# Kernel optimization log

Hardware: AMD Instinct MI355X
Metric: run time of the kernel (lower is better)

## Reference

```python
import jax, jax.numpy as jnp
import numpy as np

B_SCALE = 1.3195079565048218  # per_level_scale
N_LEVELS = 4                  # kernel hardcodes 4 levels
F = 4                         # kernel hardcodes 4 features per level
BASE = 32.0                   # kernel hardcodes base resolution 32
MAX_PARAMS = 2 ** 19
N_POINTS = 2097152


def _level_meta():
    offsets = []
    off = 0
    for i in range(N_LEVELS):
        res = int(np.ceil(BASE * np.exp(i * np.log(B_SCALE)) - 1.0)) + 1
        p = res ** 3
        p = p if p % 8 == 0 else ((p + 7) // 8) * 8
        p = min(MAX_PARAMS, p)
        offsets.append(off)
        off += p
    return offsets, off

OFFSETS, TOTAL_PARAMS = _level_meta()
TOTAL_HASH_SIZE = TOTAL_PARAMS * F  # 2772480


def setup_inputs() -> dict:
    key = jax.random.key(0)
    k1, k2 = jax.random.split(key)
    # scale to [0, 0.9) so all 8 corner indices stay inside each level's grid
    positions = jax.random.uniform(k1, (N_POINTS, 3), dtype=jnp.float32) * 0.9
    # original init: uniform(-1e-4, 1e-4); small random values
    table = jax.random.normal(k2, (TOTAL_HASH_SIZE,), dtype=jnp.float32) * 1e-4
    return {"positions": positions, "table": table}


def _encode(positions, table):
    tab = table.reshape(-1, F)  # [total_params, 4]
    n = positions.shape[0]
    outs = []
    for level in range(N_LEVELS):
        scale = BASE * (B_SCALE ** level) - 1.0
        res = int(np.ceil(scale)) + 1
        pos = positions * scale + 0.5            # [n,3]
        grid = jnp.floor(pos)
        frac = pos - grid                         # trilinear fractions
        grid = grid.astype(jnp.int32)
        acc = jnp.zeros((n, F), positions.dtype)
        for c in range(8):  # 8 corners of the cell
            w = jnp.ones((n,), positions.dtype)
            idx = jnp.zeros((n,), jnp.int32)
            stride = 1
            for d in range(3):
                if (c >> d) & 1:
                    coord = grid[:, d] + 1
                    w = w * frac[:, d]
                else:
                    coord = grid[:, d]
                    w = w * (1.0 - frac[:, d])
                idx = idx + coord * stride
                stride *= res
            acc = acc + w[:, None] * tab[OFFSETS[level] + idx]
        outs.append(acc)
    return jnp.concatenate(outs, axis=1)  # [n, 16]


def reference(positions, table):
    return _encode(positions, table)
```

## Files before the change

kernel.cpp:

```cpp
#include <hip/hip_runtime.h>
#include <math.h>


#define NBINS        512
#define BIN_SCALE    (8.0f / 0.9f)
#define SCAT_THREADS 512
#define PTS_PER_BLK  4096
#define SCAT_ITERS   (PTS_PER_BLK / SCAT_THREADS)
#define CAP          4608

#define ENC_THREADS  512
#define ENC_HALF     (CAP / 2)

#define D0 6
#define D1 7
#define D2 9
#define D3 11
#define A0 0
#define A1 (A0 + D0*D0*D0)
#define A2 (A1 + D1*D1*D1)
#define A3 (A2 + D2*D2*D2)
#define LDS_TOT (A3 + D3*D3*D3)

typedef float vfloat4 __attribute__((ext_vector_type(4)));

__device__ __forceinline__ int bin_of(float x, float y, float z) {
    int bx = (int)(x * BIN_SCALE); bx = bx < 0 ? 0 : (bx > 7 ? 7 : bx);
    int by = (int)(y * BIN_SCALE); by = by < 0 ? 0 : (by > 7 ? 7 : by);
    int bz = (int)(z * BIN_SCALE); bz = bz < 0 ? 0 : (bz > 7 ? 7 : bz);
    return bx | (by << 3) | (bz << 6);
}


__global__ __launch_bounds__(SCAT_THREADS) void scatter_cap_kernel(
    const float* __restrict__ pos, int n, int* __restrict__ cursor,
    float4* __restrict__ sorted, int bin_stride)
{
    __shared__ float4         lds_rec[PTS_PER_BLK];
    __shared__ unsigned short lds_bin[PTS_PER_BLK];
    __shared__ int lds_hist[NBINS];
    __shared__ int lds_lbase[NBINS];
    __shared__ int lds_gbase[NBINS];
    __shared__ int lds_wsum[8];

    int tid = threadIdx.x;
    long base = (long)blockIdx.x * PTS_PER_BLK;
    lds_hist[tid] = 0;
    __syncthreads();

    float px[SCAT_ITERS], py[SCAT_ITERS], pz[SCAT_ITERS];
    int br[SCAT_ITERS];
#pragma unroll
    for (int j = 0; j < SCAT_ITERS; ++j) {
        long p = base + j * SCAT_THREADS + tid;
        int packed = -1;
        if (p < n) {
            float x = pos[3 * p], y = pos[3 * p + 1], z = pos[3 * p + 2];
            px[j] = x; py[j] = y; pz[j] = z;
            int b = bin_of(x, y, z);
            int r = atomicAdd(&lds_hist[b], 1);
            packed = (r << 9) | b;
        }
        br[j] = packed;
    }
    __syncthreads();

    int lane = tid & 63, wid = tid >> 6;
    int cntb = lds_hist[tid];
    int v = cntb;
#pragma unroll
    for (int off = 1; off < 64; off <<= 1) {
        int u = __shfl_up(v, off, 64);
        if (lane >= off) v += u;
    }
    if (lane == 63) lds_wsum[wid] = v;
    __syncthreads();
    if (tid < 8) {
        int w = lds_wsum[tid];
#pragma unroll
        for (int off = 1; off < 8; off <<= 1) {
            int u = __shfl_up(w, off, 8);
            if (tid >= off) w += u;
        }
        lds_wsum[tid] = w;
    }
    if (cntb) lds_gbase[tid] = atomicAdd(&cursor[tid], cntb);
    __syncthreads();
    int wbase = wid ? lds_wsum[wid - 1] : 0;
    int excl  = wbase + v - cntb;
    lds_lbase[tid] = excl;
    __syncthreads();

#pragma unroll
    for (int j = 0; j < SCAT_ITERS; ++j) {
        if (br[j] < 0) continue;
        int b = br[j] & (NBINS - 1);
        int r = br[j] >> 9;
        int s = lds_lbase[b] + r;
        long p = base + j * SCAT_THREADS + tid;
        lds_rec[s] = make_float4(px[j], py[j], pz[j], __int_as_float((int)p));
        lds_bin[s] = (unsigned short)b;
    }
    __syncthreads();

    long rem = (long)n - base;
    int tot = rem >= PTS_PER_BLK ? PTS_PER_BLK : (rem > 0 ? (int)rem : 0);
    for (int s = tid; s < tot; s += SCAT_THREADS) {
        float4 rec = lds_rec[s];
        int b = lds_bin[s];
        int off_in_bin = s - lds_lbase[b];
        long slot = (long)b * bin_stride + lds_gbase[b] + off_in_bin;
        sorted[slot] = rec;
    }
}

template<int D>
__device__ __forceinline__ void stage_win(
    float4* __restrict__ dst, const float4* __restrict__ tab,
    int off, int res, int Bx, int By, int Bz, int tid)
{
    const int DD = D * D, DDD = D * D * D;
    for (int e = tid; e < DDD; e += ENC_THREADS) {
        int iz  = e / DD;
        int rem = e - iz * DD;
        int iy  = rem / D;
        int ix  = rem - iy * D;
        int gx = Bx + ix; gx = gx < 0 ? 0 : (gx > res - 1 ? res - 1 : gx);
        int gy = By + iy; gy = gy < 0 ? 0 : (gy > res - 1 ? res - 1 : gy);
        int gz = Bz + iz; gz = gz < 0 ? 0 : (gz > res - 1 ? res - 1 : gz);
        dst[e] = tab[off + gx + gy * res + gz * res * res];
    }
}

template<int D>
__device__ __forceinline__ float4 interp_one(
    const float4* __restrict__ lds, const float4* __restrict__ tab,
    float x, float y, float z, float scale, int res, int off,
    int Bx, int By, int Bz)
{
    float hx = x * scale + 0.5f, hy = y * scale + 0.5f, hz = z * scale + 0.5f;
    float fx = floorf(hx), fy = floorf(hy), fz = floorf(hz);
    float wx = hx - fx, wy = hy - fy, wz = hz - fz;
    float ox = 1.0f - wx, oy = 1.0f - wy, oz = 1.0f - wz;
    int gx = (int)fx, gy = (int)fy, gz = (int)fz;
    int lx = gx - Bx, ly = gy - By, lz = gz - Bz;
    float4 acc = make_float4(0.f, 0.f, 0.f, 0.f);
    if ((unsigned)lx <= (unsigned)(D - 2) &&
        (unsigned)ly <= (unsigned)(D - 2) &&
        (unsigned)lz <= (unsigned)(D - 2)) {
        int basei = (lz * D + ly) * D + lx;
#pragma unroll
        for (int c = 0; c < 8; ++c) {
            int   idx = basei + ((c & 1) ? 1 : 0) + ((c & 2) ? D : 0) + ((c & 4) ? D * D : 0);
            float w   = ((c & 1) ? wx : ox) * ((c & 2) ? wy : oy) * ((c & 4) ? wz : oz);
            float4 v  = lds[idx];
            acc.x += w * v.x; acc.y += w * v.y; acc.z += w * v.z; acc.w += w * v.w;
        }
    } else {
        int res2  = res * res;
        int basei = off + gx + gy * res + gz * res2;
#pragma unroll
        for (int c = 0; c < 8; ++c) {
            int   idx = basei + ((c & 1) ? 1 : 0) + ((c & 2) ? res : 0) + ((c & 4) ? res2 : 0);
            float w   = ((c & 1) ? wx : ox) * ((c & 2) ? wy : oy) * ((c & 4) ? wz : oz);
            float4 v  = tab[idx];
            acc.x += w * v.x; acc.y += w * v.y; acc.z += w * v.z; acc.w += w * v.w;
        }
    }
    return acc;
}

__global__ __launch_bounds__(ENC_THREADS) void encode_bin_kernel(
    const float4* __restrict__ sorted,
    const int* __restrict__ cursor,
    const float4* __restrict__ tab,
    float4* __restrict__ out,
    float s0, float s1, float s2, float s3,
    int r0, int r1, int r2, int r3,
    int o0, int o1, int o2, int o3)
{
    __shared__ float4 lds[LDS_TOT];

    int nb = (int)gridDim.x;
    int lb = (int)blockIdx.x;
    lb = (lb & 7) * (nb >> 3) + (lb >> 3);

    int b = lb >> 1;
    int k = lb & 1;
    int cnt = cursor[b];

    int begin = k * ENC_HALF;
    int end   = k ? cnt : (cnt < ENC_HALF ? cnt : ENC_HALF);
    if (begin >= end) return;

    int tid = threadIdx.x;

    int bx = b & 7, by = (b >> 3) & 7, bz = b >> 6;
    float lox = bx * 0.1125f, loy = by * 0.1125f, loz = bz * 0.1125f;

    int B0x = (int)floorf(lox * s0 + 0.5f), B0y = (int)floorf(loy * s0 + 0.5f), B0z = (int)floorf(loz * s0 + 0.5f);
    int B1x = (int)floorf(lox * s1 + 0.5f), B1y = (int)floorf(loy * s1 + 0.5f), B1z = (int)floorf(loz * s1 + 0.5f);
    int B2x = (int)floorf(lox * s2 + 0.5f), B2y = (int)floorf(loy * s2 + 0.5f), B2z = (int)floorf(loz * s2 + 0.5f);
    int B3x = (int)floorf(lox * s3 + 0.5f), B3y = (int)floorf(loy * s3 + 0.5f), B3z = (int)floorf(loz * s3 + 0.5f);

    stage_win<D0>(lds + A0, tab, o0, r0, B0x, B0y, B0z, tid);
    stage_win<D1>(lds + A1, tab, o1, r1, B1x, B1y, B1z, tid);
    stage_win<D2>(lds + A2, tab, o2, r2, B2x, B2y, B2z, tid);
    stage_win<D3>(lds + A3, tab, o3, r3, B3x, B3y, B3z, tid);
    __syncthreads();

    const float4* sbin = sorted + (long)b * CAP;
    int jmax = CAP - 1;
    int iters = (end - begin + ENC_THREADS - 1) / ENC_THREADS;

    int local = begin + tid;
    vfloat4 rv = __builtin_nontemporal_load(
        (const vfloat4*)&sbin[local <= jmax ? local : jmax]);

    for (int it = 0; it < iters; ++it) {
        int nloc = local + ENC_THREADS;
        vfloat4 nx = rv;
        if (it + 1 < iters)
            nx = __builtin_nontemporal_load(
                (const vfloat4*)&sbin[nloc <= jmax ? nloc : jmax]);
        if (local < end) {
            float x = rv.x, y = rv.y, z = rv.z;
            int p = __float_as_int(rv.w);
            float4* op = out + (long)p * 4;
            float4 a0 = interp_one<D0>(lds + A0, tab, x, y, z, s0, r0, o0, B0x, B0y, B0z);
            float4 a1 = interp_one<D1>(lds + A1, tab, x, y, z, s1, r1, o1, B1x, B1y, B1z);
            float4 a2 = interp_one<D2>(lds + A2, tab, x, y, z, s2, r2, o2, B2x, B2y, B2z);
            float4 a3 = interp_one<D3>(lds + A3, tab, x, y, z, s3, r3, o3, B3x, B3y, B3z);
            op[0] = a0; op[1] = a1; op[2] = a2; op[3] = a3;
        }
        rv = nx;
        local = nloc;
    }
}


__device__ __forceinline__ void interp_levels(
    float4 rec, const float4* __restrict__ tab, float4* __restrict__ o,
    float s0, float s1, float s2, float s3,
    int r0, int r1, int r2, int r3,
    int o0, int o1, int o2, int o3)
{
    float scales[4] = { s0, s1, s2, s3 };
    int   ress[4]   = { r0, r1, r2, r3 };
    int   offs[4]   = { o0, o1, o2, o3 };
#pragma unroll
    for (int l = 0; l < 4; ++l) {
        float scale = scales[l];
        int   res   = ress[l];
        int   off   = offs[l];
        float hx = rec.x * scale + 0.5f;
        float hy = rec.y * scale + 0.5f;
        float hz = rec.z * scale + 0.5f;
        float gx = floorf(hx), gy = floorf(hy), gz = floorf(hz);
        float wx = hx - gx,   wy = hy - gy,   wz = hz - gz;
        float ox = 1.0f - wx, oy = 1.0f - wy, oz = 1.0f - wz;
        int res2 = res * res;
        int base = off + (int)gx + (int)gy * res + (int)gz * res2;
        float4 acc = make_float4(0.f, 0.f, 0.f, 0.f);
#pragma unroll
        for (int c = 0; c < 8; ++c) {
            int   idx = base + ((c & 1) ? 1 : 0) + ((c & 2) ? res : 0) + ((c & 4) ? res2 : 0);
            float w   = ((c & 1) ? wx : ox) * ((c & 2) ? wy : oy) * ((c & 4) ? wz : oz);
            float4 v  = tab[idx];
            acc.x += w * v.x; acc.y += w * v.y; acc.z += w * v.z; acc.w += w * v.w;
        }
        o[l] = acc;
    }
}


__global__ __launch_bounds__(SCAT_THREADS) void hist_kernel(
    const float* __restrict__ pos, int n, int* __restrict__ hist)
{
    __shared__ int lh[NBINS];
    int tid = threadIdx.x;
    lh[tid] = 0;
    __syncthreads();
    long base = (long)blockIdx.x * PTS_PER_BLK;
#pragma unroll
    for (int j = 0; j < SCAT_ITERS; ++j) {
        long p = base + j * SCAT_THREADS + tid;
        if (p < n) {
            float x = pos[3 * p], y = pos[3 * p + 1], z = pos[3 * p + 2];
            atomicAdd(&lh[bin_of(x, y, z)], 1);
        }
    }
    __syncthreads();
    int c = lh[tid];
    if (c) atomicAdd(&hist[tid], c);
}

__global__ __launch_bounds__(256) void scan_kernel(
    const int* __restrict__ hist, int* __restrict__ cursor)
{
    __shared__ int partials[256];
    int t = threadIdx.x;
    int a = hist[2 * t], b = hist[2 * t + 1];
    int sum = a + b;
    partials[t] = sum;
    __syncthreads();
    for (int off = 1; off < 256; off <<= 1) {
        int v = (t >= off) ? partials[t - off] : 0;
        __syncthreads();
        partials[t] += v;
        __syncthreads();
    }
    int base = partials[t] - sum;
    cursor[2 * t]     = base;
    cursor[2 * t + 1] = base + a;
}

__global__ __launch_bounds__(256) void encode_kernel(
    const float4* __restrict__ sorted, const float4* __restrict__ tab,
    float4* __restrict__ out, int n,
    float s0, float s1, float s2, float s3,
    int r0, int r1, int r2, int r3,
    int o0, int o1, int o2, int o3)
{
    int j = blockIdx.x * blockDim.x + threadIdx.x;
    if (j >= n) return;
    vfloat4 rv = __builtin_nontemporal_load((const vfloat4*)&sorted[j]);
    float4 rec = make_float4(rv.x, rv.y, rv.z, rv.w);
    int p = __float_as_int(rec.w);
    interp_levels(rec, tab, out + (long)p * 4,
                  s0, s1, s2, s3, r0, r1, r2, r3, o0, o1, o2, o3);
}

__global__ __launch_bounds__(256) void encode_direct_kernel(
    const float* __restrict__ pos, const float4* __restrict__ tab,
    float4* __restrict__ out, int n_points,
    float s0, float s1, float s2, float s3,
    int r0, int r1, int r2, int r3,
    int o0, int o1, int o2, int o3)
{
    int t = blockIdx.x * blockDim.x + threadIdx.x;
    int p = t >> 2;
    if (p >= n_points) return;
    int l = t & 3;
    float scale = (l == 0) ? s0 : (l == 1) ? s1 : (l == 2) ? s2 : s3;
    int   res   = (l == 0) ? r0 : (l == 1) ? r1 : (l == 2) ? r2 : r3;
    int   off   = (l == 0) ? o0 : (l == 1) ? o1 : (l == 2) ? o2 : o3;
    float px = pos[3 * p], py = pos[3 * p + 1], pz = pos[3 * p + 2];
    float hx = px * scale + 0.5f, hy = py * scale + 0.5f, hz = pz * scale + 0.5f;
    float gx = floorf(hx), gy = floorf(hy), gz = floorf(hz);
    float wx = hx - gx, wy = hy - gy, wz = hz - gz;
    float ox = 1.f - wx, oy = 1.f - wy, oz = 1.f - wz;
    int res2 = res * res;
    int base = off + (int)gx + (int)gy * res + (int)gz * res2;
    float4 acc = make_float4(0.f, 0.f, 0.f, 0.f);
#pragma unroll
    for (int c = 0; c < 8; ++c) {
        int   idx = base + ((c & 1) ? 1 : 0) + ((c & 2) ? res : 0) + ((c & 4) ? res2 : 0);
        float w   = ((c & 1) ? wx : ox) * ((c & 2) ? wy : oy) * ((c & 4) ? wz : oz);
        float4 v  = tab[idx];
        acc.x += w * v.x; acc.y += w * v.y; acc.z += w * v.z; acc.w += w * v.w;
    }
    out[t] = acc;
}

extern "C" void kernel_launch(void* const* d_in, const int* in_sizes, int n_in,
                              void* d_out, int out_size, void* d_ws, size_t ws_size,
                              hipStream_t stream) {
    const float*  positions = (const float*)d_in[0];
    const float4* table     = (const float4*)d_in[1];
    float4*       out       = (float4*)d_out;
    int n = in_sizes[0] / 3;

    const double B_SCALE = 1.3195079565048218;
    const double BASE = 32.0;
    const long   MAX_PARAMS = 1L << 19;
    float scales[4]; int res[4], offs[4];
    long off = 0;
    for (int l = 0; l < 4; ++l) {
        double s = BASE * pow(B_SCALE, (double)l) - 1.0;
        scales[l] = (float)s;
        int r = (int)ceil(s) + 1;
        res[l] = r;
        offs[l] = (int)off;
        long pcount = (long)r * r * r;
        if (pcount % 8 != 0) pcount = (pcount + 7) / 8 * 8;
        if (pcount > MAX_PARAMS) pcount = MAX_PARAMS;
        off += pcount;
    }

    size_t need_cap   = (size_t)NBINS * sizeof(int) + (size_t)NBINS * CAP * 16;
    size_t need_exact = (size_t)NBINS * sizeof(int) * 2 + (size_t)n * 16;

    if (ws_size >= need_cap && n <= NBINS * (CAP - 512)) {
        int*    cursor = (int*)d_ws;
        float4* sorted = (float4*)(cursor + NBINS);

        int grid_pts = (n + PTS_PER_BLK - 1) / PTS_PER_BLK;
        int grid_enc = NBINS * 2;

        (void)hipMemsetAsync(cursor, 0, NBINS * sizeof(int), stream);
        scatter_cap_kernel<<<grid_pts, SCAT_THREADS, 0, stream>>>(
            positions, n, cursor, sorted, CAP);
        encode_bin_kernel<<<grid_enc, ENC_THREADS, 0, stream>>>(
            sorted, cursor, table, out,
            scales[0], scales[1], scales[2], scales[3],
            res[0], res[1], res[2], res[3],
            offs[0], offs[1], offs[2], offs[3]);
    } else if (ws_size >= need_exact) {
        int*    hist   = (int*)d_ws;
        int*    cursor = hist + NBINS;
        float4* sorted = (float4*)(cursor + NBINS);

        int grid_pts = (n + PTS_PER_BLK - 1) / PTS_PER_BLK;
        int grid_enc = (n + 255) / 256;

        (void)hipMemsetAsync(hist, 0, NBINS * sizeof(int), stream);
        hist_kernel<<<grid_pts, SCAT_THREADS, 0, stream>>>(positions, n, hist);
        scan_kernel<<<1, 256, 0, stream>>>(hist, cursor);
        scatter_cap_kernel<<<grid_pts, SCAT_THREADS, 0, stream>>>(
            positions, n, cursor, sorted, 0);
        encode_kernel<<<grid_enc, 256, 0, stream>>>(
            sorted, table, out, n,
            scales[0], scales[1], scales[2], scales[3],
            res[0], res[1], res[2], res[3],
            offs[0], offs[1], offs[2], offs[3]);
    } else {
        long n_threads = 4L * n;
        long grid = (n_threads + 255) / 256;
        encode_direct_kernel<<<dim3((unsigned)grid), dim3(256), 0, stream>>>(
            positions, table, out, n,
            scales[0], scales[1], scales[2], scales[3],
            res[0], res[1], res[2], res[3],
            offs[0], offs[1], offs[2], offs[3]);
    }
}
```

Measured before the change: 230.1 us.

## Sort points within each wavefront by finest-level cell before LDS interpolation

Each wavefront runs a 64-lane bitonic sort over the points it holds, keyed by their level-3 cell inside the bin window, then shuffles the coordinates so neighbouring lanes read nearby LDS entries. The aim is fewer LDS bank conflicts and more coherent gathers in interp_one. The encode grid also changes from two half-bin blocks of 512 threads to one 1024-thread block per bin. The sort adds about 21 shuffle-and-compare stages per iteration, and the larger blocks cut the number of blocks and may reduce occupancy.

```diff
diff --git a/kernel.cpp b/kernel.cpp
--- a/kernel.cpp
+++ b/kernel.cpp
@@ -9,8 +9,7 @@
 #define SCAT_ITERS   (PTS_PER_BLK / SCAT_THREADS)
 #define CAP          4608
 
-#define ENC_THREADS  512
-#define ENC_HALF     (CAP / 2)
+#define ENC_THREADS  1024
 
 #define D0 6
 #define D1 7
@@ -21,6 +20,8 @@
 #define A2 (A1 + D1*D1*D1)
 #define A3 (A2 + D2*D2*D2)
 #define LDS_TOT (A3 + D3*D3*D3)
+
+#define KEY_SENTINEL 2047u
 
 typedef float vfloat4 __attribute__((ext_vector_type(4)));
 
@@ -182,18 +183,12 @@
     __shared__ float4 lds[LDS_TOT];
 
     int nb = (int)gridDim.x;
-    int lb = (int)blockIdx.x;
-    lb = (lb & 7) * (nb >> 3) + (lb >> 3);
-
-    int b = lb >> 1;
-    int k = lb & 1;
+    int b  = (int)blockIdx.x;
+    b = (b & 7) * (nb >> 3) + (b >> 3);
+
     int cnt = cursor[b];
-
-    int begin = k * ENC_HALF;
-    int end   = k ? cnt : (cnt < ENC_HALF ? cnt : ENC_HALF);
-    if (begin >= end) return;
-
     int tid = threadIdx.x;
+    int lane = tid & 63;
 
     int bx = b & 7, by = (b >> 3) & 7, bz = b >> 6;
     float lox = bx * 0.1125f, loy = by * 0.1125f, loz = bz * 0.1125f;
@@ -209,11 +204,15 @@
     stage_win<D3>(lds + A3, tab, o3, r3, B3x, B3y, B3z, tid);
     __syncthreads();
 
+    if (cnt == 0) return;
+
+    int iters = (cnt + ENC_THREADS - 1) / ENC_THREADS;
     const float4* sbin = sorted + (long)b * CAP;
     int jmax = CAP - 1;
-    int iters = (end - begin + ENC_THREADS - 1) / ENC_THREADS;
-
-    int local = begin + tid;
+
+    float cx = lox + 0.05625f, cy = loy + 0.05625f, cz = loz + 0.05625f;
+
+    int local = tid;
     vfloat4 rv = __builtin_nontemporal_load(
         (const vfloat4*)&sbin[local <= jmax ? local : jmax]);
 
@@ -223,14 +222,46 @@
         if (it + 1 < iters)
             nx = __builtin_nontemporal_load(
                 (const vfloat4*)&sbin[nloc <= jmax ? nloc : jmax]);
-        if (local < end) {
-            float x = rv.x, y = rv.y, z = rv.z;
-            int p = __float_as_int(rv.w);
+
+        bool valid = (local < cnt);
+        float x = valid ? rv.x : cx;
+        float y = valid ? rv.y : cy;
+        float z = valid ? rv.z : cz;
+        float pw = rv.w;
+
+        int kx = (int)floorf(x * s3 + 0.5f) - B3x; kx = kx < 0 ? 0 : (kx > D3 - 1 ? D3 - 1 : kx);
+        int ky = (int)floorf(y * s3 + 0.5f) - B3y; ky = ky < 0 ? 0 : (ky > D3 - 1 ? D3 - 1 : ky);
+        int kz = (int)floorf(z * s3 + 0.5f) - B3z; kz = kz < 0 ? 0 : (kz > D3 - 1 ? D3 - 1 : kz);
+        unsigned key = valid ? (unsigned)((kz * D3 + ky) * D3 + kx) : KEY_SENTINEL;
+        unsigned comp = (key << 6) | (unsigned)lane;
+
+#pragma unroll
+        for (int k = 2; k <= 64; k <<= 1) {
+#pragma unroll
+            for (int j = k >> 1; j >= 1; j >>= 1) {
+                unsigned o = (unsigned)__shfl_xor((int)comp, j, 64);
+                bool up    = ((lane & k) == 0);
+                bool lower = ((lane & j) == 0);
+                unsigned mn = comp < o ? comp : o;
+                unsigned mx = comp < o ? o : comp;
+                comp = (lower == up) ? mn : mx;
+            }
+        }
+        int src = (int)(comp & 63u);
+        x  = __shfl(x,  src, 64);
+        y  = __shfl(y,  src, 64);
+        z  = __shfl(z,  src, 64);
+        pw = __shfl(pw, src, 64);
+        valid = ((comp >> 6) != KEY_SENTINEL);
+
+        float4 a0 = interp_one<D0>(lds + A0, tab, x, y, z, s0, r0, o0, B0x, B0y, B0z);
+        float4 a1 = interp_one<D1>(lds + A1, tab, x, y, z, s1, r1, o1, B1x, B1y, B1z);
+        float4 a2 = interp_one<D2>(lds + A2, tab, x, y, z, s2, r2, o2, B2x, B2y, B2z);
+        float4 a3 = interp_one<D3>(lds + A3, tab, x, y, z, s3, r3, o3, B3x, B3y, B3z);
+
+        if (valid) {
+            int p = __float_as_int(pw);
             float4* op = out + (long)p * 4;
-            float4 a0 = interp_one<D0>(lds + A0, tab, x, y, z, s0, r0, o0, B0x, B0y, B0z);
-            float4 a1 = interp_one<D1>(lds + A1, tab, x, y, z, s1, r1, o1, B1x, B1y, B1z);
-            float4 a2 = interp_one<D2>(lds + A2, tab, x, y, z, s2, r2, o2, B2x, B2y, B2z);
-            float4 a3 = interp_one<D3>(lds + A3, tab, x, y, z, s3, r3, o3, B3x, B3y, B3z);
             op[0] = a0; op[1] = a1; op[2] = a2; op[3] = a3;
         }
         rv = nx;
@@ -396,12 +427,11 @@
         float4* sorted = (float4*)(cursor + NBINS);
 
         int grid_pts = (n + PTS_PER_BLK - 1) / PTS_PER_BLK;
-        int grid_enc = NBINS * 2;
 
         (void)hipMemsetAsync(cursor, 0, NBINS * sizeof(int), stream);
         scatter_cap_kernel<<<grid_pts, SCAT_THREADS, 0, stream>>>(
             positions, n, cursor, sorted, CAP);
-        encode_bin_kernel<<<grid_enc, ENC_THREADS, 0, stream>>>(
+        encode_bin_kernel<<<NBINS, ENC_THREADS, 0, stream>>>(
             sorted, cursor, table, out,
             scales[0], scales[1], scales[2], scales[3],
             res[0], res[1], res[2], res[3],
```

After: 230.4 us. Within noise of the previous version (+0.1%).

## Vectorize scatter position loads and use one 1024-thread encode block per bin

Applied to the files above, without the earlier changes.

The scatter kernel now has each thread load four consecutive points as three float4 vector loads, replacing scalar strided loads, which should improve coalescing on the positions read. The encode kernel goes from two 512-thread blocks per bin (each handling half of the bin) to a single 1024-thread block per bin. This halves the number of times each bin's table window is staged into LDS. The trade-off is fewer blocks in flight and a larger block that may limit occupancy, and the vector path assumes 16-byte alignment of the positions buffer.

```diff
diff --git a/kernel.cpp b/kernel.cpp
--- a/kernel.cpp
+++ b/kernel.cpp
@@ -7,10 +7,11 @@
 #define SCAT_THREADS 512
 #define PTS_PER_BLK  4096
 #define SCAT_ITERS   (PTS_PER_BLK / SCAT_THREADS)
+#define PTS_PER_PASS (SCAT_THREADS * 4)
+#define NPASS        (PTS_PER_BLK / PTS_PER_PASS)
 #define CAP          4608
 
-#define ENC_THREADS  512
-#define ENC_HALF     (CAP / 2)
+#define ENC_THREADS  1024
 
 #define D0 6
 #define D1 7
@@ -48,20 +49,40 @@
     lds_hist[tid] = 0;
     __syncthreads();
 
-    float px[SCAT_ITERS], py[SCAT_ITERS], pz[SCAT_ITERS];
-    int br[SCAT_ITERS];
-#pragma unroll
-    for (int j = 0; j < SCAT_ITERS; ++j) {
-        long p = base + j * SCAT_THREADS + tid;
-        int packed = -1;
-        if (p < n) {
-            float x = pos[3 * p], y = pos[3 * p + 1], z = pos[3 * p + 2];
-            px[j] = x; py[j] = y; pz[j] = z;
-            int b = bin_of(x, y, z);
-            int r = atomicAdd(&lds_hist[b], 1);
-            packed = (r << 9) | b;
-        }
-        br[j] = packed;
+    float px[4 * NPASS], py[4 * NPASS], pz[4 * NPASS];
+    int br[4 * NPASS];
+#pragma unroll
+    for (int pass = 0; pass < NPASS; ++pass) {
+        long p0 = base + (long)pass * PTS_PER_PASS + 4 * tid;
+        int ii = pass * 4;
+        if (p0 + 4 <= n) {
+            const float4* v = (const float4*)(pos + 3 * p0);
+            float4 A = v[0], B = v[1], C = v[2];
+            px[ii+0]=A.x; py[ii+0]=A.y; pz[ii+0]=A.z;
+            px[ii+1]=A.w; py[ii+1]=B.x; pz[ii+1]=B.y;
+            px[ii+2]=B.z; py[ii+2]=B.w; pz[ii+2]=C.x;
+            px[ii+3]=C.y; py[ii+3]=C.z; pz[ii+3]=C.w;
+#pragma unroll
+            for (int q = 0; q < 4; ++q) {
+                int b = bin_of(px[ii+q], py[ii+q], pz[ii+q]);
+                int r = atomicAdd(&lds_hist[b], 1);
+                br[ii+q] = (r << 9) | b;
+            }
+        } else {
+#pragma unroll
+            for (int q = 0; q < 4; ++q) {
+                long p = p0 + q;
+                int packed = -1;
+                if (p < n) {
+                    float x = pos[3*p], y = pos[3*p+1], z = pos[3*p+2];
+                    px[ii+q]=x; py[ii+q]=y; pz[ii+q]=z;
+                    int b = bin_of(x, y, z);
+                    int r = atomicAdd(&lds_hist[b], 1);
+                    packed = (r << 9) | b;
+                }
+                br[ii+q] = packed;
+            }
+        }
     }
     __syncthreads();
 
@@ -92,13 +113,13 @@
     __syncthreads();
 
 #pragma unroll
-    for (int j = 0; j < SCAT_ITERS; ++j) {
-        if (br[j] < 0) continue;
-        int b = br[j] & (NBINS - 1);
-        int r = br[j] >> 9;
+    for (int ii = 0; ii < 4 * NPASS; ++ii) {
+        if (br[ii] < 0) continue;
+        int b = br[ii] & (NBINS - 1);
+        int r = br[ii] >> 9;
         int s = lds_lbase[b] + r;
-        long p = base + j * SCAT_THREADS + tid;
-        lds_rec[s] = make_float4(px[j], py[j], pz[j], __int_as_float((int)p));
+        long p = base + (long)(ii >> 2) * PTS_PER_PASS + 4 * tid + (ii & 3);
+        lds_rec[s] = make_float4(px[ii], py[ii], pz[ii], __int_as_float((int)p));
         lds_bin[s] = (unsigned short)b;
     }
     __syncthreads();
@@ -182,17 +203,10 @@
     __shared__ float4 lds[LDS_TOT];
 
     int nb = (int)gridDim.x;
-    int lb = (int)blockIdx.x;
-    lb = (lb & 7) * (nb >> 3) + (lb >> 3);
-
-    int b = lb >> 1;
-    int k = lb & 1;
+    int b  = (int)blockIdx.x;
+    b = (b & 7) * (nb >> 3) + (b >> 3);
+
     int cnt = cursor[b];
-
-    int begin = k * ENC_HALF;
-    int end   = k ? cnt : (cnt < ENC_HALF ? cnt : ENC_HALF);
-    if (begin >= end) return;
-
     int tid = threadIdx.x;
 
     int bx = b & 7, by = (b >> 3) & 7, bz = b >> 6;
@@ -209,11 +223,13 @@
     stage_win<D3>(lds + A3, tab, o3, r3, B3x, B3y, B3z, tid);
     __syncthreads();
 
+    if (cnt == 0) return;
+
+    int iters = (cnt + ENC_THREADS - 1) / ENC_THREADS;
     const float4* sbin = sorted + (long)b * CAP;
     int jmax = CAP - 1;
-    int iters = (end - begin + ENC_THREADS - 1) / ENC_THREADS;
-
-    int local = begin + tid;
+
+    int local = tid;
     vfloat4 rv = __builtin_nontemporal_load(
         (const vfloat4*)&sbin[local <= jmax ? local : jmax]);
 
@@ -223,7 +239,7 @@
         if (it + 1 < iters)
             nx = __builtin_nontemporal_load(
                 (const vfloat4*)&sbin[nloc <= jmax ? nloc : jmax]);
-        if (local < end) {
+        if (local < cnt) {
             float x = rv.x, y = rv.y, z = rv.z;
             int p = __float_as_int(rv.w);
             float4* op = out + (long)p * 4;
@@ -396,12 +412,11 @@
         float4* sorted = (float4*)(cursor + NBINS);
 
         int grid_pts = (n + PTS_PER_BLK - 1) / PTS_PER_BLK;
-        int grid_enc = NBINS * 2;
 
         (void)hipMemsetAsync(cursor, 0, NBINS * sizeof(int), stream);
         scatter_cap_kernel<<<grid_pts, SCAT_THREADS, 0, stream>>>(
             positions, n, cursor, sorted, CAP);
-        encode_bin_kernel<<<grid_enc, ENC_THREADS, 0, stream>>>(
+        encode_bin_kernel<<<NBINS, ENC_THREADS, 0, stream>>>(
             sorted, cursor, table, out,
             scales[0], scales[1], scales[2], scales[3],
             res[0], res[1], res[2], res[3],
```

After: 223.4 us. -2.9%, faster.
